# Kernel optimization log

Measured on AMD Instinct MI355X. Metric: run time of the kernel, lower is better.

The kernel has to match this reference:

```python
import jax, jax.numpy as jnp
import numpy as np
import math

B, L, D_MODEL = 4, 2048, 32
H, F = 2, 16  # num_heads, feature_dim (== head_dim)
RD = math.sqrt(F)          # sqrt(input_dim) = 4
R2 = math.sqrt(2.0)
RRD = math.sqrt(RD)        # = 2


def setup_inputs() -> dict:
    key = jax.random.key(0)
    ks = jax.random.split(key, 5)
    s = 1.0 / math.sqrt(D_MODEL)
    return {
        "hidden_states": jax.random.normal(ks[0], (B, L, D_MODEL), jnp.float32),
        "Wq": jax.random.normal(ks[1], (D_MODEL, H * F), jnp.float32) * s,
        "Wk": jax.random.normal(ks[2], (D_MODEL, H * F), jnp.float32) * s,
        "Wv": jax.random.normal(ks[3], (D_MODEL, H * F), jnp.float32) * s,
        "Wo": jax.random.normal(ks[4], (H * F, D_MODEL), jnp.float32) * s,
    }


def _lin_attn(Q, K, V):
    # Q,K,V: [b,h,n,d] with d=f=e=16. Taylor-series linear attention, causal.
    b, h, n, d = Q.shape
    # 2nd-order term
    A2 = jnp.cumsum(jnp.einsum('bhnd,bhnf,bhne->bhndef', K, V, K), axis=2) / (RD * R2)
    Q2 = jnp.einsum('bhnd,bhne->bhnde', Q, Q) / (RD * R2)
    T2 = jnp.einsum('bhnde,bhndef->bhnf', Q2, A2)
    # 1st-order term
    A1 = jnp.cumsum(jnp.einsum('bhnd,bhne->bhnde', K, V), axis=2) / RRD
    T1 = jnp.einsum('bhnd,bhnde->bhne', Q / RRD, A1)
    # 0th-order term
    T0 = jnp.cumsum(V, axis=2)
    # denominators
    K2cs = jnp.cumsum(jnp.einsum('bhnd,bhne->bhnde', K, K), axis=2) / (RD * R2)
    D2 = jnp.einsum('bhnde,bhnde->bhn', Q2, K2cs)
    D1 = jnp.einsum('bhnd,bhnd->bhn', Q, jnp.cumsum(K, axis=2)) / (RRD ** 2)
    D0 = jnp.broadcast_to(jnp.arange(1, n + 1, dtype=Q.dtype), (b, h, n))
    numerator = T0 + T1 + T2
    denominator = D0 + D1 + D2
    return numerator / denominator[..., None]  # [b,h,n,f]


def reference(hidden_states, Wq, Wk, Wv, Wo):
    b, l, _ = hidden_states.shape
    q = (hidden_states @ Wq).reshape(b, l, H, F).transpose(0, 2, 1, 3)
    k = (hidden_states @ Wk).reshape(b, l, H, F).transpose(0, 2, 1, 3)
    v = (hidden_states @ Wv).reshape(b, l, H, F).transpose(0, 2, 1, 3)
    y = _lin_attn(q, k, v)                       # [b,h,l,f]
    y = y.transpose(0, 2, 1, 3).reshape(b, l, H * F)  # b l (h d)
    return y @ Wo
```

## Files before the change

### kernel.cpp

```cpp
#include <hip/hip_runtime.h>

#define L_SEQ 2048
#define NH 2
#define FD 16
#define BH 8
#define QT 32
#define NT 64
#define SCW 128

typedef _Float16 half4f __attribute__((ext_vector_type(4)));
typedef float floatx4 __attribute__((ext_vector_type(4)));

struct FalseT { static constexpr bool value = false; };
struct TrueT  { static constexpr bool value = true;  };

__global__ __launch_bounds__(256) void qkv_proj_kernel(
    const float* __restrict__ hs, const float* __restrict__ Wq,
    const float* __restrict__ Wk, const float* __restrict__ Wv,
    _Float16* __restrict__ q, _Float16* __restrict__ k,
    _Float16* __restrict__ v) {
  __shared__ float sW[3][32][32];
  __shared__ float sH[32][32];
  int tid = threadIdx.x;
  float* swf = &sW[0][0][0];
  for (int i = tid; i < 3072; i += 256)
    swf[i] = (i < 1024) ? Wq[i] : (i < 2048) ? Wk[i - 1024] : Wv[i - 2048];
  int row0 = blockIdx.x * 32;
  int r0 = tid >> 5, c = tid & 31;
  for (int p = 0; p < 4; p++) {
    int r = r0 + p * 8;
    sH[r][c] = hs[(size_t)(row0 + r) * 32 + c];
  }
  __syncthreads();
  int hh = c >> 4, f = c & 15;
  for (int p = 0; p < 4; p++) {
    int r = r0 + p * 8;
    float aq = 0.f, ak = 0.f, av = 0.f;
#pragma unroll
    for (int i = 0; i < 32; i++) {
      float h = sH[r][i];
      aq += h * sW[0][i][c];
      ak += h * sW[1][i][c];
      av += h * sW[2][i][c];
    }
    int row = row0 + r;
    int b = row >> 11, l = row & (L_SEQ - 1);
    size_t idx = (((size_t)(b * NH + hh)) * L_SEQ + l) * FD + f;
    q[idx] = (_Float16)(aq * 0.25f);
    k[idx] = (_Float16)ak;
    v[idx] = (_Float16)av;
  }
}

__global__ __launch_bounds__(256) void attn_fused_kernel(
    const _Float16* __restrict__ q, const _Float16* __restrict__ k,
    const _Float16* __restrict__ v, const float* __restrict__ Wo,
    float* __restrict__ out) {
  __shared__ _Float16 sK[NH][128][24];
  __shared__ _Float16 sVT[NH][16][136];
  __shared__ float sDen[4][16];
  __shared__ float sY[QT][33];
  __shared__ float sWo[32][32];

  int tid = threadIdx.x;
  int b = blockIdx.y;
  int t = NT - 1 - (int)blockIdx.x;
  int lane = tid & 63;
  int wid = tid >> 6;
  int lm = lane & 15, lg = lane >> 4;
  int h = wid >> 1, sub = wid & 1;
  int bh = b * NH + h;

  for (int i = tid; i < 1024; i += 256) (&sWo[0][0])[i] = Wo[i];

  int q0 = t * QT + sub * 16;
  half4f qf = *(const half4f*)(q + ((size_t)bh * L_SEQ + q0 + lm) * FD + 4 * lg);

  floatx4 o = (floatx4){0.f, 0.f, 0.f, 0.f};
  float dn = 0.f;
  int tq = q0 + lm;
  int lastc = t >> 2;
  int ss = tid >> 1, hf = tid & 1;

  auto body = [&](int sc, auto mc) {
    constexpr bool MASK = decltype(mc)::value;
    int sb = sc * SCW + 4 * lg;
#pragma unroll
    for (int st = 0; st < 8; st++) {
      half4f kf = *(const half4f*)&sK[h][st * 16 + lm][4 * lg];
      half4f vf = *(const half4f*)&sVT[h][lm][st * 16 + 4 * lg];
      floatx4 sT = __builtin_amdgcn_mfma_f32_16x16x16f16(
          kf, qf, (floatx4){0.f, 0.f, 0.f, 0.f}, 0, 0, 0);
      float wvv[4];
#pragma unroll
      for (int r = 0; r < 4; r++) {
        float a = sT[r];
        float wr = (0.5f * a + 1.f) * a + 1.f;
        if (MASK) wr = (sb + st * 16 + r <= tq) ? wr : 0.f;
        wvv[r] = wr;
        dn += wr;
      }
      half4f wf = {(_Float16)wvv[0], (_Float16)wvv[1],
                   (_Float16)wvv[2], (_Float16)wvv[3]};
      o = __builtin_amdgcn_mfma_f32_16x16x16f16(wf, vf, o, 0, 0, 0);
    }
  };

  for (int sc = 0; sc <= lastc; sc++) {
    __syncthreads();
#pragma unroll
    for (int hh = 0; hh < NH; hh++) {
      const _Float16* kp =
          k + (((size_t)(b * NH + hh)) * L_SEQ + sc * SCW + ss) * FD + 8 * hf;
      const _Float16* vp =
          v + (((size_t)(b * NH + hh)) * L_SEQ + sc * SCW + ss) * FD + 8 * hf;
      *(uint4*)&sK[hh][ss][8 * hf] = *(const uint4*)kp;
      union { uint4 u; _Float16 e[8]; } vu;
      vu.u = *(const uint4*)vp;
#pragma unroll
      for (int i = 0; i < 8; i++) sVT[hh][8 * hf + i][ss] = vu.e[i];
    }
    __syncthreads();
    if (sc < lastc) body(sc, FalseT{}); else body(sc, TrueT{});
  }

  dn += __shfl_xor(dn, 16, 64);
  dn += __shfl_xor(dn, 32, 64);
  if (lg == 0) sDen[wid][lm] = dn;
  __syncthreads();
#pragma unroll
  for (int r = 0; r < 4; r++) {
    float dd = sDen[wid][4 * lg + r];
    sY[sub * 16 + 4 * lg + r][h * 16 + lm] = o[r] / dd;
  }
  __syncthreads();

  int c = tid & 31, r0 = tid >> 5;
  float wo[32];
#pragma unroll
  for (int i = 0; i < 32; i++) wo[i] = sWo[i][c];
#pragma unroll
  for (int p = 0; p < 4; p++) {
    int r = r0 + p * 8;
    float a = 0.f;
#pragma unroll
    for (int i = 0; i < 32; i++) a += sY[r][i] * wo[i];
    out[((size_t)b * L_SEQ + t * QT + r) * 32 + c] = a;
  }
}

extern "C" void kernel_launch(void* const* d_in, const int* in_sizes, int n_in,
                              void* d_out, int out_size, void* d_ws, size_t ws_size,
                              hipStream_t stream) {
  const float* hs = (const float*)d_in[0];
  const float* Wq = (const float*)d_in[1];
  const float* Wk = (const float*)d_in[2];
  const float* Wv = (const float*)d_in[3];
  const float* Wo = (const float*)d_in[4];
  float* out = (float*)d_out;

  char* wb = (char*)d_ws;
  const size_t PER = (size_t)BH * L_SEQ * FD;
  _Float16* qh = (_Float16*)wb;
  _Float16* kh = qh + PER;
  _Float16* vh = kh + PER;

  qkv_proj_kernel<<<256, 256, 0, stream>>>(hs, Wq, Wk, Wv, qh, kh, vh);
  attn_fused_kernel<<<dim3(NT, 4), 256, 0, stream>>>(qh, kh, vh, Wo, out);
}
```

Baseline: 87.77 us.

## Split key chunks across wave pairs with partial-sum reduction in attention kernel

Each wave now handles both 16-query sub-tiles for one head and half of the key chunks, alternating chunk parity. Two chunks are loaded per round into double shared buffers, and the per-wave partial outputs and denominators are combined through shared memory at the end. The goal is to halve the number of sequential chunk iterations and barriers per block and to reuse each K/V fragment load for two queries. The cost is more shared memory, extra registers and a cross-wave reduction step, and the final round leaves one wave idle when the chunk count is odd.

Result: no change. 87.78 us (+0.0%).

```diff
diff --git a/kernel.cpp b/kernel.cpp
--- a/kernel.cpp
+++ b/kernel.cpp
@@ -56,9 +56,10 @@
     const _Float16* __restrict__ q, const _Float16* __restrict__ k,
     const _Float16* __restrict__ v, const float* __restrict__ Wo,
     float* __restrict__ out) {
-  __shared__ _Float16 sK[NH][128][24];
-  __shared__ _Float16 sVT[NH][16][136];
-  __shared__ float sDen[4][16];
+  __shared__ _Float16 sK[2][NH][128][24];
+  __shared__ _Float16 sVT[2][NH][16][136];
+  __shared__ float sO[2][NH][2][16][17];
+  __shared__ float sDen[2][NH][2][16];
   __shared__ float sY[QT][33];
   __shared__ float sWo[32][32];
 
@@ -68,17 +69,28 @@
   int lane = tid & 63;
   int wid = tid >> 6;
   int lm = lane & 15, lg = lane >> 4;
-  int h = wid >> 1, sub = wid & 1;
+  int h = wid >> 1, par = wid & 1;
   int bh = b * NH + h;
 
   for (int i = tid; i < 1024; i += 256) (&sWo[0][0])[i] = Wo[i];
 
-  int q0 = t * QT + sub * 16;
-  half4f qf = *(const half4f*)(q + ((size_t)bh * L_SEQ + q0 + lm) * FD + 4 * lg);
-
-  floatx4 o = (floatx4){0.f, 0.f, 0.f, 0.f};
-  float dn = 0.f;
-  int tq = q0 + lm;
+  half4f qf[2];
+#pragma unroll
+  for (int sub = 0; sub < 2; sub++)
+    qf[sub] = *(const half4f*)(
+        q + ((size_t)bh * L_SEQ + t * QT + sub * 16 + lm) * FD + 4 * lg);
+
+  floatx4 o[2];
+  float dn[2];
+#pragma unroll
+  for (int i = 0; i < 2; i++) {
+    o[i] = (floatx4){0.f, 0.f, 0.f, 0.f};
+    dn[i] = 0.f;
+  }
+  int tq[2];
+#pragma unroll
+  for (int sub = 0; sub < 2; sub++) tq[sub] = t * QT + sub * 16 + lm;
+
   int lastc = t >> 2;
   int ss = tid >> 1, hf = tid & 1;
 
@@ -87,51 +99,83 @@
     int sb = sc * SCW + 4 * lg;
 #pragma unroll
     for (int st = 0; st < 8; st++) {
-      half4f kf = *(const half4f*)&sK[h][st * 16 + lm][4 * lg];
-      half4f vf = *(const half4f*)&sVT[h][lm][st * 16 + 4 * lg];
-      floatx4 sT = __builtin_amdgcn_mfma_f32_16x16x16f16(
-          kf, qf, (floatx4){0.f, 0.f, 0.f, 0.f}, 0, 0, 0);
-      float wvv[4];
-#pragma unroll
-      for (int r = 0; r < 4; r++) {
-        float a = sT[r];
-        float wr = (0.5f * a + 1.f) * a + 1.f;
-        if (MASK) wr = (sb + st * 16 + r <= tq) ? wr : 0.f;
-        wvv[r] = wr;
-        dn += wr;
+      half4f kf = *(const half4f*)&sK[par][h][st * 16 + lm][4 * lg];
+      half4f vf = *(const half4f*)&sVT[par][h][lm][st * 16 + 4 * lg];
+#pragma unroll
+      for (int sub = 0; sub < 2; sub++) {
+        floatx4 sT = __builtin_amdgcn_mfma_f32_16x16x16f16(
+            kf, qf[sub], (floatx4){0.f, 0.f, 0.f, 0.f}, 0, 0, 0);
+        float wvv[4];
+#pragma unroll
+        for (int r = 0; r < 4; r++) {
+          float a = sT[r];
+          float wr = (0.5f * a + 1.f) * a + 1.f;
+          if (MASK) wr = (sb + st * 16 + r <= tq[sub]) ? wr : 0.f;
+          wvv[r] = wr;
+          dn[sub] += wr;
+        }
+        half4f wf = {(_Float16)wvv[0], (_Float16)wvv[1],
+                     (_Float16)wvv[2], (_Float16)wvv[3]};
+        o[sub] = __builtin_amdgcn_mfma_f32_16x16x16f16(wf, vf, o[sub], 0, 0, 0);
       }
-      half4f wf = {(_Float16)wvv[0], (_Float16)wvv[1],
-                   (_Float16)wvv[2], (_Float16)wvv[3]};
-      o = __builtin_amdgcn_mfma_f32_16x16x16f16(wf, vf, o, 0, 0, 0);
     }
   };
 
-  for (int sc = 0; sc <= lastc; sc++) {
+  int nr = (lastc >> 1) + 1;
+  for (int rd = 0; rd < nr; rd++) {
+    int c0 = rd * 2;
     __syncthreads();
 #pragma unroll
-    for (int hh = 0; hh < NH; hh++) {
-      const _Float16* kp =
-          k + (((size_t)(b * NH + hh)) * L_SEQ + sc * SCW + ss) * FD + 8 * hf;
-      const _Float16* vp =
-          v + (((size_t)(b * NH + hh)) * L_SEQ + sc * SCW + ss) * FD + 8 * hf;
-      *(uint4*)&sK[hh][ss][8 * hf] = *(const uint4*)kp;
-      union { uint4 u; _Float16 e[8]; } vu;
-      vu.u = *(const uint4*)vp;
-#pragma unroll
-      for (int i = 0; i < 8; i++) sVT[hh][8 * hf + i][ss] = vu.e[i];
+    for (int p = 0; p < 2; p++) {
+      int c = c0 + p;
+      if (c <= lastc) {
+#pragma unroll
+        for (int hh = 0; hh < NH; hh++) {
+          const _Float16* kp =
+              k + (((size_t)(b * NH + hh)) * L_SEQ + c * SCW + ss) * FD + 8 * hf;
+          const _Float16* vp =
+              v + (((size_t)(b * NH + hh)) * L_SEQ + c * SCW + ss) * FD + 8 * hf;
+          *(uint4*)&sK[p][hh][ss][8 * hf] = *(const uint4*)kp;
+          union { uint4 u; _Float16 e[8]; } vu;
+          vu.u = *(const uint4*)vp;
+#pragma unroll
+          for (int i = 0; i < 8; i++) sVT[p][hh][8 * hf + i][ss] = vu.e[i];
+        }
+      }
     }
     __syncthreads();
-    if (sc < lastc) body(sc, FalseT{}); else body(sc, TrueT{});
-  }
-
-  dn += __shfl_xor(dn, 16, 64);
-  dn += __shfl_xor(dn, 32, 64);
-  if (lg == 0) sDen[wid][lm] = dn;
+    int c = c0 + par;
+    if (c <= lastc) {
+      if (c < lastc) body(c, FalseT{}); else body(c, TrueT{});
+    }
+  }
+
+#pragma unroll
+  for (int sub = 0; sub < 2; sub++) {
+    dn[sub] += __shfl_xor(dn[sub], 16, 64);
+    dn[sub] += __shfl_xor(dn[sub], 32, 64);
+  }
+  if (lg == 0) {
+    sDen[par][h][0][lm] = dn[0];
+    sDen[par][h][1][lm] = dn[1];
+  }
+#pragma unroll
+  for (int sub = 0; sub < 2; sub++)
+#pragma unroll
+    for (int r = 0; r < 4; r++)
+      sO[par][h][sub][4 * lg + r][lm] = o[sub][r];
   __syncthreads();
-#pragma unroll
-  for (int r = 0; r < 4; r++) {
-    float dd = sDen[wid][4 * lg + r];
-    sY[sub * 16 + 4 * lg + r][h * 16 + lm] = o[r] / dd;
+
+  {
+    int q32 = tid >> 3, cb = (tid & 7) * 4;
+    int subq = q32 >> 4, qrow = q32 & 15;
+    int hc = cb >> 4, fb = cb & 15;
+    float dtot = sDen[0][hc][subq][qrow] + sDen[1][hc][subq][qrow];
+    float inv = 1.f / dtot;
+#pragma unroll
+    for (int j = 0; j < 4; j++)
+      sY[q32][cb + j] =
+          (sO[0][hc][subq][qrow][fb + j] + sO[1][hc][subq][qrow][fb + j]) * inv;
   }
   __syncthreads();
 
```
